# Kernel tuning notes

Hardware: AMD Instinct MI355X
Metric: run time of the kernel (lower is better)

Reference implementation:

```python
import jax, jax.numpy as jnp
import numpy as np

B, S, D = 8, 1024, 768
H = 12
HD = D // H  # 64
SCALE = 1.0 / (HD ** 0.5)


def setup_inputs() -> dict:
    key = jax.random.key(0)
    ks = jax.random.split(key, 5)
    x = jax.random.normal(ks[0], (B, S, D), dtype=jnp.float32)
    W_qkv = jax.random.normal(ks[1], (D, 3 * D), dtype=jnp.float32) * 0.02
    b_qkv = jax.random.normal(ks[2], (3 * D,), dtype=jnp.float32) * 0.02
    W_proj = jax.random.normal(ks[3], (D, D), dtype=jnp.float32) * 0.02
    b_proj = jax.random.normal(ks[4], (D,), dtype=jnp.float32) * 0.02
    return {"x": x, "W_qkv": W_qkv, "b_qkv": b_qkv, "W_proj": W_proj, "b_proj": b_proj}


def reference(x, W_qkv, b_qkv, W_proj, b_proj):
    b, s, d = x.shape
    # QKV projection: (B, S, 3D) -> (3, B, H, S, HD)
    qkv = x @ W_qkv + b_qkv
    qkv = qkv.reshape(b, s, 3, H, HD).transpose(2, 0, 3, 1, 4)
    q, k, v = qkv[0], qkv[1], qkv[2]
    # scaled dot-product attention (full matrix, as in the original)
    scores = jnp.einsum("bhqd,bhkd->bhqk", q, k) * SCALE
    attn = jax.nn.softmax(scores, axis=-1)
    out = jnp.einsum("bhqk,bhkd->bhqd", attn, v)
    # merge heads: (B, S, D)
    out = out.transpose(0, 2, 1, 3).reshape(b, s, d)
    return out @ W_proj + b_proj
```

## Files before the change

kernel.cpp:

```cpp
#include <hip/hip_runtime.h>
#include <math.h>

typedef __attribute__((ext_vector_type(8))) unsigned short ushortx8;
typedef __attribute__((ext_vector_type(8))) __bf16 bf16x8;
typedef __attribute__((ext_vector_type(4))) float floatx4;
typedef __attribute__((ext_vector_type(16))) float floatx16;

#define NH 12
#define SEQ 1024
#define DM 768
#define HD 64
#define GK 768
#define QK_SCALE 0.18033688011112042f

#define GLDS16(gp, lp) __builtin_amdgcn_global_load_lds( \
    (const __attribute__((address_space(1))) unsigned int*)(const void*)(gp), \
    (__attribute__((address_space(3))) unsigned int*)(lp), 16, 0, 0)

__device__ __forceinline__ unsigned short f2bf(float f) {
    union { float f; unsigned u; } v; v.f = f;
    unsigned r = v.u + 0x7fffu + ((v.u >> 16) & 1u);
    return (unsigned short)(r >> 16);
}

__device__ __forceinline__ unsigned pk2bf(float f0, float f1) {
    union { float f; unsigned u; } a, b; a.f = f0; b.f = f1;
    return ((a.u + 0x8000u) >> 16) | ((b.u + 0x8000u) & 0xffff0000u);
}

__device__ __forceinline__ void mfma_block(const unsigned short* Ab, const unsigned short* Bb,
                                           int wr, int wc, int l15, int quad, floatx4 acc[4][4]) {
    bf16x8 af[4], bfr[4];
#pragma unroll
    for (int mt = 0; mt < 4; mt++)
        af[mt] = __builtin_bit_cast(bf16x8, *(const ushortx8*)&Ab[(wr * 64 + mt * 16 + l15) * 32 + quad * 8]);
#pragma unroll
    for (int nt = 0; nt < 4; nt++)
        bfr[nt] = __builtin_bit_cast(bf16x8, *(const ushortx8*)&Bb[(wc * 64 + nt * 16 + l15) * 32 + quad * 8]);
#pragma unroll
    for (int mt = 0; mt < 4; mt++)
#pragma unroll
        for (int nt = 0; nt < 4; nt++)
            acc[mt][nt] = __builtin_amdgcn_mfma_f32_16x16x32_bf16(af[mt], bfr[nt], acc[mt][nt], 0, 0, 0);
}

__global__ void k_prep(const float* __restrict__ x, unsigned short* __restrict__ x_bf,
                       const float* __restrict__ Wqkv, unsigned short* __restrict__ WqkvT,
                       const float* __restrict__ Wproj, unsigned short* __restrict__ WprojT) {
    __shared__ float tile[32][33];
    int bx = blockIdx.x;
    if (bx < 6144) {
        int i = bx * 256 + threadIdx.x;
        float4 v = ((const float4*)x)[i];
        ushort4 o;
        o.x = f2bf(v.x); o.y = f2bf(v.y); o.z = f2bf(v.z); o.w = f2bf(v.w);
        ((ushort4*)x_bf)[i] = o;
        return;
    }
    const float* in; unsigned short* out; int R, C, c0, r0;
    if (bx < 7872) {
        int t = bx - 6144;
        in = Wqkv; out = WqkvT; R = 768; C = 2304;
        c0 = (t % 72) * 32; r0 = (t / 72) * 32;
    } else {
        int t = bx - 7872;
        in = Wproj; out = WprojT; R = 768; C = 768;
        c0 = (t % 24) * 32; r0 = (t / 24) * 32;
    }
    int tx = threadIdx.x & 31, ty = threadIdx.x >> 5;
#pragma unroll
    for (int i = 0; i < 4; i++)
        tile[ty + 8 * i][tx] = in[(size_t)(r0 + ty + 8 * i) * C + c0 + tx];
    __syncthreads();
#pragma unroll
    for (int i = 0; i < 4; i++)
        out[(size_t)(c0 + ty + 8 * i) * R + r0 + tx] = f2bf(tile[tx][ty + 8 * i]);
}

__global__ __launch_bounds__(256) void k_gemm_qkv(
    const unsigned short* __restrict__ A, const unsigned short* __restrict__ Bt,
    const float* __restrict__ bias,
    unsigned short* __restrict__ Qb, unsigned short* __restrict__ Kb,
    unsigned short* __restrict__ Vt) {
    __shared__ unsigned short smem[17408];
    unsigned short* As0 = smem;
    unsigned short* Bs0 = smem + 4096;
    unsigned short* As1 = smem + 8192;
    unsigned short* Bs1 = smem + 12288;
    int tid = threadIdx.x;
    int w = tid >> 6, lane = tid & 63;
    int quad = lane >> 4, l15 = lane & 15;
    int wr = w >> 1, wc = w & 1;
    int lin = blockIdx.x;
    int xcd = lin & 7, slot = lin >> 3;
    int mt_i = xcd * 8 + (slot & 7);
    int nt_i = slot >> 3;
    int m0 = mt_i * 128, n0 = nt_i * 128;

    int r = lane >> 2, c = (lane & 3) * 8;
    const unsigned short* gA0 = A + (size_t)(m0 + w * 32 + r) * GK + c;
    const unsigned short* gA1 = A + (size_t)(m0 + w * 32 + 16 + r) * GK + c;
    const unsigned short* gB0 = Bt + (size_t)(n0 + w * 32 + r) * GK + c;
    const unsigned short* gB1 = Bt + (size_t)(n0 + w * 32 + 16 + r) * GK + c;
    unsigned short* lA0a = &As0[(w * 32) * 32];
    unsigned short* lA0b = &As0[(w * 32 + 16) * 32];
    unsigned short* lB0a = &Bs0[(w * 32) * 32];
    unsigned short* lB0b = &Bs0[(w * 32 + 16) * 32];
    unsigned short* lA1a = &As1[(w * 32) * 32];
    unsigned short* lA1b = &As1[(w * 32 + 16) * 32];
    unsigned short* lB1a = &Bs1[(w * 32) * 32];
    unsigned short* lB1b = &Bs1[(w * 32 + 16) * 32];

    floatx4 acc[4][4] = {};
    GLDS16(gA0, lA0a);
    GLDS16(gA1, lA0b);
    GLDS16(gB0, lB0a);
    GLDS16(gB1, lB0b);
    for (int k0 = 0; k0 < GK; k0 += 64) {
        __syncthreads();
        {
            int kn = k0 + 32;
            GLDS16(gA0 + kn, lA1a);
            GLDS16(gA1 + kn, lA1b);
            GLDS16(gB0 + kn, lB1a);
            GLDS16(gB1 + kn, lB1b);
        }
        mfma_block(As0, Bs0, wr, wc, l15, quad, acc);
        __syncthreads();
        if (k0 + 64 < GK) {
            int kn = k0 + 64;
            GLDS16(gA0 + kn, lA0a);
            GLDS16(gA1 + kn, lA0b);
            GLDS16(gB0 + kn, lB0a);
            GLDS16(gB1 + kn, lB0b);
        }
        mfma_block(As1, Bs1, wr, wc, l15, quad, acc);
    }

    int tsel = nt_i / 6;
    int bb = m0 >> 10;
    int s_base0 = (m0 & 1023) + wr * 64;
    if (tsel < 2) {
#pragma unroll
        for (int mt = 0; mt < 4; mt++) {
            int s_base = s_base0 + mt * 16 + quad * 4;
#pragma unroll
            for (int nt = 0; nt < 4; nt++) {
                int n_g = n0 + wc * 64 + nt * 16 + l15;
                int nloc = n_g - tsel * 768;
                int hh = nloc >> 6, dd = nloc & 63;
                float bv = bias[n_g];
                if (tsel == 0) {
#pragma unroll
                    for (int rg = 0; rg < 4; rg++)
                        Qb[((size_t)(bb * NH + hh) * SEQ + s_base + rg) * HD + dd] =
                            f2bf((acc[mt][nt][rg] + bv) * QK_SCALE);
                } else {
#pragma unroll
                    for (int rg = 0; rg < 4; rg++)
                        Kb[((size_t)(bb * NH + hh) * SEQ + s_base + rg) * HD + dd] =
                            f2bf(acc[mt][nt][rg] + bv);
                }
            }
        }
    } else {
        __syncthreads();
#pragma unroll
        for (int mt = 0; mt < 4; mt++) {
#pragma unroll
            for (int nt = 0; nt < 4; nt++) {
                int n_g = n0 + wc * 64 + nt * 16 + l15;
                float bv = bias[n_g];
                int rowr = wc * 64 + nt * 16 + l15;
                ushort4 pk;
                pk.x = f2bf(acc[mt][nt][0] + bv);
                pk.y = f2bf(acc[mt][nt][1] + bv);
                pk.z = f2bf(acc[mt][nt][2] + bv);
                pk.w = f2bf(acc[mt][nt][3] + bv);
                *(ushort4*)&smem[rowr * 136 + wr * 64 + mt * 16 + quad * 4] = pk;
            }
        }
        __syncthreads();
        int row = tid >> 1, half = tid & 1;
        int head0 = (n0 - 1536) >> 6;
        int hh = head0 + (row >> 6), dd = row & 63;
        size_t gbase = ((size_t)(bb * NH + hh) * HD + dd) * SEQ + (m0 & 1023) + half * 64;
#pragma unroll
        for (int i = 0; i < 8; i++)
            *(uint4*)&Vt[gbase + i * 8] = *(const uint4*)&smem[row * 136 + half * 64 + i * 8];
    }
}

__global__ __launch_bounds__(256) void k_attn(
    const unsigned short* __restrict__ Qb, const unsigned short* __restrict__ Kb,
    const unsigned short* __restrict__ Vt, unsigned short* __restrict__ attn_out) {
    __shared__ unsigned short Ks[64 * 72];
    __shared__ unsigned short Vts[64 * 72];
    __shared__ unsigned short Pt[4][32 * 72];
    int tid = threadIdx.x;
    int w = tid >> 6, lane = tid & 63;
    int l31 = lane & 31, lh = lane >> 5;
    int lin = blockIdx.x;
    int xcd = lin & 7, slot = lin >> 3;
    int bh = xcd * 12 + (slot >> 3);
    int qt = slot & 7;
    int b = bh / NH, h = bh - b * NH;
    const unsigned short* Qp = Qb + (size_t)bh * SEQ * HD;
    const unsigned short* Kp = Kb + (size_t)bh * SEQ * HD;
    const unsigned short* Vp = Vt + (size_t)bh * HD * SEQ;
    int q0w = qt * 128 + w * 32;
    unsigned short* Ptw = &Pt[w][0];

    bf16x8 qf[4];
#pragma unroll
    for (int ds = 0; ds < 4; ds++)
        qf[ds] = __builtin_bit_cast(bf16x8,
            *(const ushortx8*)&Qp[(size_t)(q0w + l31) * HD + ds * 16 + lh * 8]);

    floatx16 o[2] = {};
    float lsum = 0.f;

    int rr = tid >> 3, cc8 = (tid & 7) * 8;
    uint4 kr0 = *(const uint4*)&Kp[(size_t)rr * HD + cc8];
    uint4 kr1 = *(const uint4*)&Kp[(size_t)(rr + 32) * HD + cc8];
    uint4 vr0 = *(const uint4*)&Vp[(size_t)rr * SEQ + cc8];
    uint4 vr1 = *(const uint4*)&Vp[(size_t)(rr + 32) * SEQ + cc8];

    for (int kb = 0; kb < SEQ; kb += 64) {
        __syncthreads();
        *(uint4*)&Ks[rr * 72 + cc8] = kr0;
        *(uint4*)&Ks[(rr + 32) * 72 + cc8] = kr1;
        *(uint4*)&Vts[rr * 72 + cc8] = vr0;
        *(uint4*)&Vts[(rr + 32) * 72 + cc8] = vr1;
        if (kb + 64 < SEQ) {
            kr0 = *(const uint4*)&Kp[(size_t)(kb + 64 + rr) * HD + cc8];
            kr1 = *(const uint4*)&Kp[(size_t)(kb + 64 + rr + 32) * HD + cc8];
            vr0 = *(const uint4*)&Vp[(size_t)rr * SEQ + kb + 64 + cc8];
            vr1 = *(const uint4*)&Vp[(size_t)(rr + 32) * SEQ + kb + 64 + cc8];
        }
        __syncthreads();

        floatx16 sc[2] = {};
#pragma unroll
        for (int mt = 0; mt < 2; mt++)
#pragma unroll
            for (int ds = 0; ds < 4; ds++) {
                bf16x8 kf = __builtin_bit_cast(bf16x8,
                    *(const ushortx8*)&Ks[(mt * 32 + l31) * 72 + ds * 16 + lh * 8]);
                sc[mt] = __builtin_amdgcn_mfma_f32_32x32x16_bf16(kf, qf[ds], sc[mt], 0, 0, 0);
            }

#pragma unroll
        for (int mt = 0; mt < 2; mt++)
#pragma unroll
            for (int g = 0; g < 4; g++) {
                float p0 = exp2f(sc[mt][g * 4 + 0]);
                float p1 = exp2f(sc[mt][g * 4 + 1]);
                float p2 = exp2f(sc[mt][g * 4 + 2]);
                float p3 = exp2f(sc[mt][g * 4 + 3]);
                lsum += (p0 + p1) + (p2 + p3);
                uint2 pk;
                pk.x = pk2bf(p0, p1);
                pk.y = pk2bf(p2, p3);
                *(uint2*)&Ptw[l31 * 72 + mt * 32 + g * 8 + lh * 4] = pk;
            }

#pragma unroll
        for (int ks = 0; ks < 4; ks++) {
            bf16x8 pf = __builtin_bit_cast(bf16x8,
                *(const ushortx8*)&Ptw[l31 * 72 + ks * 16 + lh * 8]);
#pragma unroll
            for (int mt = 0; mt < 2; mt++) {
                bf16x8 vf = __builtin_bit_cast(bf16x8,
                    *(const ushortx8*)&Vts[(mt * 32 + l31) * 72 + ks * 16 + lh * 8]);
                o[mt] = __builtin_amdgcn_mfma_f32_32x32x16_bf16(vf, pf, o[mt], 0, 0, 0);
            }
        }
    }

    lsum += __shfl_xor(lsum, 32, 64);
    float inv = 1.0f / lsum;

#pragma unroll
    for (int mt = 0; mt < 2; mt++)
#pragma unroll
        for (int g = 0; g < 4; g++) {
            uint2 pk;
            pk.x = pk2bf(o[mt][g * 4 + 0] * inv, o[mt][g * 4 + 1] * inv);
            pk.y = pk2bf(o[mt][g * 4 + 2] * inv, o[mt][g * 4 + 3] * inv);
            *(uint2*)&Ptw[l31 * 72 + mt * 32 + g * 8 + lh * 4] = pk;
        }
#pragma unroll
    for (int pass = 0; pass < 4; pass++) {
        int row = pass * 8 + (lane >> 3);
        int col8 = (lane & 7) * 8;
        uint4 vv = *(const uint4*)&Ptw[row * 72 + col8];
        *(uint4*)&attn_out[(size_t)(b * SEQ + q0w + row) * DM + h * HD + col8] = vv;
    }
}

__global__ __launch_bounds__(256) void k_gemm_proj(
    const unsigned short* __restrict__ A, const unsigned short* __restrict__ Bt,
    const float* __restrict__ bias, float* __restrict__ out) {
    __shared__ unsigned short smem[16384];
    unsigned short* As0 = smem;
    unsigned short* Bs0 = smem + 4096;
    unsigned short* As1 = smem + 8192;
    unsigned short* Bs1 = smem + 12288;
    int tid = threadIdx.x;
    int w = tid >> 6, lane = tid & 63;
    int quad = lane >> 4, l15 = lane & 15;
    int wr = w >> 1, wc = w & 1;
    int lin = blockIdx.x;
    int xcd = lin & 7, slot = lin >> 3;
    int mt_i = xcd * 8 + (slot & 7);
    int nt_i = slot >> 3;
    int m0 = mt_i * 128, n0 = nt_i * 128;

    int r = lane >> 2, c = (lane & 3) * 8;
    const unsigned short* gA0 = A + (size_t)(m0 + w * 32 + r) * GK + c;
    const unsigned short* gA1 = A + (size_t)(m0 + w * 32 + 16 + r) * GK + c;
    const unsigned short* gB0 = Bt + (size_t)(n0 + w * 32 + r) * GK + c;
    const unsigned short* gB1 = Bt + (size_t)(n0 + w * 32 + 16 + r) * GK + c;
    unsigned short* lA0a = &As0[(w * 32) * 32];
    unsigned short* lA0b = &As0[(w * 32 + 16) * 32];
    unsigned short* lB0a = &Bs0[(w * 32) * 32];
    unsigned short* lB0b = &Bs0[(w * 32 + 16) * 32];
    unsigned short* lA1a = &As1[(w * 32) * 32];
    unsigned short* lA1b = &As1[(w * 32 + 16) * 32];
    unsigned short* lB1a = &Bs1[(w * 32) * 32];
    unsigned short* lB1b = &Bs1[(w * 32 + 16) * 32];

    floatx4 acc[4][4] = {};
    GLDS16(gA0, lA0a);
    GLDS16(gA1, lA0b);
    GLDS16(gB0, lB0a);
    GLDS16(gB1, lB0b);
    for (int k0 = 0; k0 < GK; k0 += 64) {
        __syncthreads();
        {
            int kn = k0 + 32;
            GLDS16(gA0 + kn, lA1a);
            GLDS16(gA1 + kn, lA1b);
            GLDS16(gB0 + kn, lB1a);
            GLDS16(gB1 + kn, lB1b);
        }
        mfma_block(As0, Bs0, wr, wc, l15, quad, acc);
        __syncthreads();
        if (k0 + 64 < GK) {
            int kn = k0 + 64;
            GLDS16(gA0 + kn, lA0a);
            GLDS16(gA1 + kn, lA0b);
            GLDS16(gB0 + kn, lB0a);
            GLDS16(gB1 + kn, lB0b);
        }
        mfma_block(As1, Bs1, wr, wc, l15, quad, acc);
    }

#pragma unroll
    for (int mt = 0; mt < 4; mt++) {
        int m_base = m0 + wr * 64 + mt * 16 + quad * 4;
#pragma unroll
        for (int nt = 0; nt < 4; nt++) {
            int n_g = n0 + wc * 64 + nt * 16 + l15;
            float bv = bias[n_g];
#pragma unroll
            for (int rg = 0; rg < 4; rg++)
                out[(size_t)(m_base + rg) * DM + n_g] = acc[mt][nt][rg] + bv;
        }
    }
}

extern "C" void kernel_launch(void* const* d_in, const int* in_sizes, int n_in,
                              void* d_out, int out_size, void* d_ws, size_t ws_size,
                              hipStream_t stream) {
    const float* x     = (const float*)d_in[0];
    const float* Wqkv  = (const float*)d_in[1];
    const float* bqkv  = (const float*)d_in[2];
    const float* Wproj = (const float*)d_in[3];
    const float* bproj = (const float*)d_in[4];
    float* out = (float*)d_out;

    char* ws = (char*)d_ws;
    unsigned short* x_bf   = (unsigned short*)(ws);
    unsigned short* WqkvT  = (unsigned short*)(ws + 12582912);
    unsigned short* WprojT = (unsigned short*)(ws + 16121856);
    unsigned short* Qb     = (unsigned short*)(ws + 17301504);
    unsigned short* Kb     = (unsigned short*)(ws + 29884416);
    unsigned short* Vt     = (unsigned short*)(ws + 42467328);
    unsigned short* attn   = (unsigned short*)(ws + 55050240);

    k_prep<<<8448, 256, 0, stream>>>(x, x_bf, Wqkv, WqkvT, Wproj, WprojT);
    k_gemm_qkv<<<1152, 256, 0, stream>>>(x_bf, WqkvT, bqkv, Qb, Kb, Vt);
    k_attn<<<768, 256, 0, stream>>>(Qb, Kb, Vt, attn);
    k_gemm_proj<<<384, 256, 0, stream>>>(attn, WprojT, bproj, out);
}
```

Measured before the change: 204.4 us.

## Enlarge QKV GEMM tiles to 256x256 with 512 threads and deeper K staging

Rewrites the QKV projection GEMM to use 256x256 output tiles per 512-thread block with 64-wide K stages, double-buffered in 128KB of LDS, explicit vmcnt waits, raw barriers and s_setprio around MFMA phases. This raises arithmetic intensity and cuts redundant global loads and barrier count compared with the 128x128 tiles. The grid shrinks to 288 blocks, which may underfill the 256 CUs and leaves only one block per CU because of the LDS use. The V transpose epilogue is split into two halves so it fits the staging buffer.

Result: slower. 238.4 us (+16.6%).

```diff
diff --git a/kernel.cpp b/kernel.cpp
--- a/kernel.cpp
+++ b/kernel.cpp
@@ -77,117 +77,142 @@
         out[(size_t)(c0 + ty + 8 * i) * R + r0 + tx] = f2bf(tile[tx][ty + 8 * i]);
 }
 
-__global__ __launch_bounds__(256) void k_gemm_qkv(
+
+__device__ __forceinline__ void qkv_stage(const unsigned short* gA, const unsigned short* gB,
+                                          unsigned short* lbuf, int w, int k0) {
+#pragma unroll
+    for (int r = 0; r < 4; r++) {
+        int cid = r * 8 + w;
+        int kk = cid >> 4, sr = cid & 15;
+        GLDS16(gA + (size_t)sr * 16 * GK + k0 + kk * 32, lbuf + kk * 8192 + sr * 512);
+        GLDS16(gB + (size_t)sr * 16 * GK + k0 + kk * 32, lbuf + 16384 + kk * 8192 + sr * 512);
+    }
+}
+
+__device__ __forceinline__ void qkv_phase(const unsigned short* Ab, const unsigned short* Bb,
+                                          int wm, int wn, int l15, int quad, int qm, int qn,
+                                          floatx4 (&acc)[8][4]) {
+    bf16x8 af[4][2], bfr[2][2];
+#pragma unroll
+    for (int m = 0; m < 4; m++)
+#pragma unroll
+        for (int k = 0; k < 2; k++)
+            af[m][k] = __builtin_bit_cast(bf16x8,
+                *(const ushortx8*)&Ab[k * 8192 + (wm * 128 + qm * 64 + m * 16 + l15) * 32 + quad * 8]);
+#pragma unroll
+    for (int n = 0; n < 2; n++)
+#pragma unroll
+        for (int k = 0; k < 2; k++)
+            bfr[n][k] = __builtin_bit_cast(bf16x8,
+                *(const ushortx8*)&Bb[k * 8192 + (wn * 64 + qn * 32 + n * 16 + l15) * 32 + quad * 8]);
+    __builtin_amdgcn_s_setprio(1);
+#pragma unroll
+    for (int m = 0; m < 4; m++)
+#pragma unroll
+        for (int n = 0; n < 2; n++)
+#pragma unroll
+            for (int k = 0; k < 2; k++)
+                acc[qm * 4 + m][qn * 2 + n] = __builtin_amdgcn_mfma_f32_16x16x32_bf16(
+                    af[m][k], bfr[n][k], acc[qm * 4 + m][qn * 2 + n], 0, 0, 0);
+    __builtin_amdgcn_s_setprio(0);
+    __builtin_amdgcn_s_barrier();
+    asm volatile("" ::: "memory");
+}
+
+__global__ __launch_bounds__(512, 2) void k_gemm_qkv(
     const unsigned short* __restrict__ A, const unsigned short* __restrict__ Bt,
     const float* __restrict__ bias,
     unsigned short* __restrict__ Qb, unsigned short* __restrict__ Kb,
     unsigned short* __restrict__ Vt) {
-    __shared__ unsigned short smem[17408];
-    unsigned short* As0 = smem;
-    unsigned short* Bs0 = smem + 4096;
-    unsigned short* As1 = smem + 8192;
-    unsigned short* Bs1 = smem + 12288;
+    __shared__ unsigned short smem[65536];
     int tid = threadIdx.x;
     int w = tid >> 6, lane = tid & 63;
     int quad = lane >> 4, l15 = lane & 15;
-    int wr = w >> 1, wc = w & 1;
+    int wm = w >> 2, wn = w & 3;
     int lin = blockIdx.x;
     int xcd = lin & 7, slot = lin >> 3;
-    int mt_i = xcd * 8 + (slot & 7);
-    int nt_i = slot >> 3;
-    int m0 = mt_i * 128, n0 = nt_i * 128;
-
-    int r = lane >> 2, c = (lane & 3) * 8;
-    const unsigned short* gA0 = A + (size_t)(m0 + w * 32 + r) * GK + c;
-    const unsigned short* gA1 = A + (size_t)(m0 + w * 32 + 16 + r) * GK + c;
-    const unsigned short* gB0 = Bt + (size_t)(n0 + w * 32 + r) * GK + c;
-    const unsigned short* gB1 = Bt + (size_t)(n0 + w * 32 + 16 + r) * GK + c;
-    unsigned short* lA0a = &As0[(w * 32) * 32];
-    unsigned short* lA0b = &As0[(w * 32 + 16) * 32];
-    unsigned short* lB0a = &Bs0[(w * 32) * 32];
-    unsigned short* lB0b = &Bs0[(w * 32 + 16) * 32];
-    unsigned short* lA1a = &As1[(w * 32) * 32];
-    unsigned short* lA1b = &As1[(w * 32 + 16) * 32];
-    unsigned short* lB1a = &Bs1[(w * 32) * 32];
-    unsigned short* lB1b = &Bs1[(w * 32 + 16) * 32];
-
-    floatx4 acc[4][4] = {};
-    GLDS16(gA0, lA0a);
-    GLDS16(gA1, lA0b);
-    GLDS16(gB0, lB0a);
-    GLDS16(gB1, lB0b);
-    for (int k0 = 0; k0 < GK; k0 += 64) {
-        __syncthreads();
-        {
-            int kn = k0 + 32;
-            GLDS16(gA0 + kn, lA1a);
-            GLDS16(gA1 + kn, lA1b);
-            GLDS16(gB0 + kn, lB1a);
-            GLDS16(gB1 + kn, lB1b);
-        }
-        mfma_block(As0, Bs0, wr, wc, l15, quad, acc);
-        __syncthreads();
-        if (k0 + 64 < GK) {
-            int kn = k0 + 64;
-            GLDS16(gA0 + kn, lA0a);
-            GLDS16(gA1 + kn, lA0b);
-            GLDS16(gB0 + kn, lB0a);
-            GLDS16(gB1 + kn, lB0b);
-        }
-        mfma_block(As1, Bs1, wr, wc, l15, quad, acc);
-    }
-
-    int tsel = nt_i / 6;
+    int tile = xcd * 36 + slot;
+    int nt_i = tile >> 5;
+    int mt_i = tile & 31;
+    int m0 = mt_i * 256, n0 = nt_i * 256;
+
+    int rA = lane >> 2, cA = (lane & 3) * 8;
+    const unsigned short* gAbase = A + (size_t)(m0 + rA) * GK + cA;
+    const unsigned short* gBbase = Bt + (size_t)(n0 + rA) * GK + cA;
+
+    floatx4 acc[8][4] = {};
+
+    qkv_stage(gAbase, gBbase, smem, w, 0);
+    qkv_stage(gAbase, gBbase, smem + 32768, w, 64);
+#pragma unroll 1
+    for (int t = 0; t < 12; t++) {
+        if (t == 11) asm volatile("s_waitcnt vmcnt(0)" ::: "memory");
+        else         asm volatile("s_waitcnt vmcnt(8)" ::: "memory");
+        __builtin_amdgcn_s_barrier();
+        asm volatile("" ::: "memory");
+        const unsigned short* Ab = smem + (t & 1) * 32768;
+        const unsigned short* Bb = Ab + 16384;
+        qkv_phase(Ab, Bb, wm, wn, l15, quad, 0, 0, acc);
+        qkv_phase(Ab, Bb, wm, wn, l15, quad, 0, 1, acc);
+        qkv_phase(Ab, Bb, wm, wn, l15, quad, 1, 0, acc);
+        qkv_phase(Ab, Bb, wm, wn, l15, quad, 1, 1, acc);
+        if (t < 10) qkv_stage(gAbase, gBbase, smem + (t & 1) * 32768, w, (t + 2) * 64);
+    }
+
+    int tsel = nt_i / 3;
     int bb = m0 >> 10;
-    int s_base0 = (m0 & 1023) + wr * 64;
+    int s_base0 = (m0 & 1023) + wm * 128;
     if (tsel < 2) {
-#pragma unroll
-        for (int mt = 0; mt < 4; mt++) {
+        unsigned short* __restrict__ dst = (tsel == 0) ? Qb : Kb;
+#pragma unroll
+        for (int mt = 0; mt < 8; mt++) {
             int s_base = s_base0 + mt * 16 + quad * 4;
 #pragma unroll
             for (int nt = 0; nt < 4; nt++) {
-                int n_g = n0 + wc * 64 + nt * 16 + l15;
+                int n_g = n0 + wn * 64 + nt * 16 + l15;
                 int nloc = n_g - tsel * 768;
                 int hh = nloc >> 6, dd = nloc & 63;
                 float bv = bias[n_g];
+                size_t base = ((size_t)(bb * NH + hh) * SEQ + s_base) * HD + dd;
                 if (tsel == 0) {
 #pragma unroll
                     for (int rg = 0; rg < 4; rg++)
-                        Qb[((size_t)(bb * NH + hh) * SEQ + s_base + rg) * HD + dd] =
-                            f2bf((acc[mt][nt][rg] + bv) * QK_SCALE);
+                        dst[base + (size_t)rg * HD] = f2bf((acc[mt][nt][rg] + bv) * QK_SCALE);
                 } else {
 #pragma unroll
                     for (int rg = 0; rg < 4; rg++)
-                        Kb[((size_t)(bb * NH + hh) * SEQ + s_base + rg) * HD + dd] =
-                            f2bf(acc[mt][nt][rg] + bv);
+                        dst[base + (size_t)rg * HD] = f2bf(acc[mt][nt][rg] + bv);
                 }
             }
         }
     } else {
-        __syncthreads();
-#pragma unroll
-        for (int mt = 0; mt < 4; mt++) {
-#pragma unroll
-            for (int nt = 0; nt < 4; nt++) {
-                int n_g = n0 + wc * 64 + nt * 16 + l15;
-                float bv = bias[n_g];
-                int rowr = wc * 64 + nt * 16 + l15;
-                ushort4 pk;
-                pk.x = f2bf(acc[mt][nt][0] + bv);
-                pk.y = f2bf(acc[mt][nt][1] + bv);
-                pk.z = f2bf(acc[mt][nt][2] + bv);
-                pk.w = f2bf(acc[mt][nt][3] + bv);
-                *(ushort4*)&smem[rowr * 136 + wr * 64 + mt * 16 + quad * 4] = pk;
+        int head0 = (n0 - 1536) >> 6;
+        for (int mh = 0; mh < 2; mh++) {
+            __syncthreads();
+            if (wm == mh) {
+#pragma unroll
+                for (int mt = 0; mt < 8; mt++) {
+#pragma unroll
+                    for (int nt = 0; nt < 4; nt++) {
+                        int col = wn * 64 + nt * 16 + l15;
+                        float bv = bias[n0 + col];
+                        ushort4 pk;
+                        pk.x = f2bf(acc[mt][nt][0] + bv);
+                        pk.y = f2bf(acc[mt][nt][1] + bv);
+                        pk.z = f2bf(acc[mt][nt][2] + bv);
+                        pk.w = f2bf(acc[mt][nt][3] + bv);
+                        *(ushort4*)&smem[col * 136 + mt * 16 + quad * 4] = pk;
+                    }
+                }
             }
-        }
-        __syncthreads();
-        int row = tid >> 1, half = tid & 1;
-        int head0 = (n0 - 1536) >> 6;
-        int hh = head0 + (row >> 6), dd = row & 63;
-        size_t gbase = ((size_t)(bb * NH + hh) * HD + dd) * SEQ + (m0 & 1023) + half * 64;
-#pragma unroll
-        for (int i = 0; i < 8; i++)
-            *(uint4*)&Vt[gbase + i * 8] = *(const uint4*)&smem[row * 136 + half * 64 + i * 8];
+            __syncthreads();
+            int col = tid >> 1, part = tid & 1;
+            int hh = head0 + (col >> 6), dd = col & 63;
+            size_t gbase = ((size_t)(bb * NH + hh) * HD + dd) * SEQ + (m0 & 1023) + mh * 128 + part * 64;
+#pragma unroll
+            for (int i = 0; i < 8; i++)
+                *(uint4*)&Vt[gbase + i * 8] = *(const uint4*)&smem[col * 136 + part * 64 + i * 8];
+        }
     }
 }
 
@@ -391,7 +416,7 @@
     unsigned short* attn   = (unsigned short*)(ws + 55050240);
 
     k_prep<<<8448, 256, 0, stream>>>(x, x_bf, Wqkv, WqkvT, Wproj, WprojT);
-    k_gemm_qkv<<<1152, 256, 0, stream>>>(x_bf, WqkvT, bqkv, Qb, Kb, Vt);
+    k_gemm_qkv<<<288, 512, 0, stream>>>(x_bf, WqkvT, bqkv, Qb, Kb, Vt);
     k_attn<<<768, 256, 0, stream>>>(Qb, Kb, Vt, attn);
     k_gemm_proj<<<384, 256, 0, stream>>>(attn, WprojT, bproj, out);
 }
```
